# Optimization experiments

Hardware: AMD Instinct MI355X
Metric: run time of the kernel (lower is better)

Reference implementation:

```python
import jax, jax.numpy as jnp
import numpy as np

HS = [192, 96, 48, 24, 12, 6]
WS = [384, 192, 96, 48, 24, 12]
C = 64    # feature channels per pyramid level
F = 64    # num_features (conv output channels)
CIN = 2 * C + 2  # current + warped + 2 flow channels = 130
N = 4


def dense_image_warp(image, flow):
    """tfa.image.dense_image_warp: warped[b,y,x] = bilinear(image[b, y - flow_y, x - flow_x]).
    Boundary handling matches tfa._interpolate_bilinear: floor indices clipped to
    [0, size-2], interpolation alphas clipped to [0, 1]."""
    n, h, w, _ = image.shape
    gy, gx = jnp.meshgrid(jnp.arange(h, dtype=flow.dtype),
                          jnp.arange(w, dtype=flow.dtype), indexing='ij')
    qy = gy[None] - flow[..., 0]          # [N,H,W] query rows
    qx = gx[None] - flow[..., 1]          # [N,H,W] query cols
    y0 = jnp.clip(jnp.floor(qy), 0, h - 2).astype(jnp.int32)
    x0 = jnp.clip(jnp.floor(qx), 0, w - 2).astype(jnp.int32)
    ay = jnp.clip(qy - y0.astype(flow.dtype), 0.0, 1.0)[..., None]
    ax = jnp.clip(qx - x0.astype(flow.dtype), 0.0, 1.0)[..., None]
    b = jnp.arange(n)[:, None, None]
    tl = image[b, y0, x0]
    tr = image[b, y0, x0 + 1]
    bl = image[b, y0 + 1, x0]
    br = image[b, y0 + 1, x0 + 1]
    top = tl + (tr - tl) * ax
    bot = bl + (br - bl) * ax
    return top + (bot - top) * ay


def separable_conv1x1(x, dw, pw, bias):
    # SeparableConv2D with 1x1 kernel: depthwise per-channel scale, then pointwise matmul.
    return jnp.einsum('nhwc,cf->nhwf', x * dw, pw) + bias


def _forward(xcs, xps, fls, dws, pws, bs):
    outs = []
    for i in range(6):
        # _warp: dense_image_warp(x_prev, -flow)
        warped = dense_image_warp(xps[i], -fls[i])
        x = jnp.concatenate([xcs[i], warped, fls[i]], axis=-1)  # [N,H,W,130]
        outs.append(separable_conv1x1(x, dws[i], pws[i], bs[i]))
    return tuple(outs)


def setup_inputs() -> dict:
    key = jax.random.key(0)
    d = {}
    for i in range(6):
        h, w = HS[i], WS[i]
        ks = jax.random.split(jax.random.fold_in(key, i), 6)
        d[f'xc{i}'] = jax.random.normal(ks[0], (N, h, w, C), jnp.float32)
        d[f'xp{i}'] = jax.random.normal(ks[1], (N, h, w, C), jnp.float32)
        d[f'fl{i}'] = jax.random.normal(ks[2], (N, h, w, 2), jnp.float32) * 2.0
        d[f'dw{i}'] = jax.random.normal(ks[3], (CIN,), jnp.float32) * 0.1
        d[f'pw{i}'] = jax.random.normal(ks[4], (CIN, F), jnp.float32) * 0.05
        d[f'bias{i}'] = jnp.zeros((F,), jnp.float32)
    return d


def reference(xc0, xc1, xc2, xc3, xc4, xc5,
              xp0, xp1, xp2, xp3, xp4, xp5,
              fl0, fl1, fl2, fl3, fl4, fl5,
              dw0, dw1, dw2, dw3, dw4, dw5,
              pw0, pw1, pw2, pw3, pw4, pw5,
              bias0, bias1, bias2, bias3, bias4, bias5):
    xcs = (xc0, xc1, xc2, xc3, xc4, xc5)
    xps = (xp0, xp1, xp2, xp3, xp4, xp5)
    fls = (fl0, fl1, fl2, fl3, fl4, fl5)
    dws = (dw0, dw1, dw2, dw3, dw4, dw5)
    pws = (pw0, pw1, pw2, pw3, pw4, pw5)
    bs = (bias0, bias1, bias2, bias3, bias4, bias5)
    return _forward(xcs, xps, fls, dws, pws, bs)
```

## Files before the change

kernel.cpp:

```cpp
#include <hip/hip_runtime.h>


typedef __attribute__((ext_vector_type(8))) short bf16x8;
typedef __attribute__((ext_vector_type(4))) float f32x4;

#define WS_LVL_STRIDE 17408

__device__ inline unsigned rne_bf16_bits(float f) {
  unsigned u = __builtin_bit_cast(unsigned, f);
  u += 0x7fffu + ((u >> 16) & 1u);
  return u >> 16;
}
__device__ inline int pack_bf16x2(float a, float b) {
  return (int)(rne_bf16_bits(a) | (rne_bf16_bits(b) << 16));
}

struct LevelArgs {
  const float* __restrict__ xc;
  const float* __restrict__ xp;
  const float* __restrict__ fl;
  float* __restrict__ out;
  const char* __restrict__ wsl;
  int H, W, npix, block_start;
};
struct KArgs { LevelArgs lv[6]; int total_blocks; };

struct PrepLevel {
  const float* __restrict__ dw;
  const float* __restrict__ pw;
  const float* __restrict__ bias;
  char* __restrict__ wsl;
};
struct PrepArgs { PrepLevel lv[6]; };

__global__ void prep_kernel(PrepArgs pa) {
  const PrepLevel P = pa.lv[blockIdx.x];
  int4* __restrict__ frag = (int4*)P.wsl;
  for (int e = (int)threadIdx.x; e < 1024; e += 256) {
    const int kt = e >> 8;
    const int nt = (e >> 6) & 3;
    const int lane = e & 63;
    const int n = 4 * (lane & 15) + nt;
    const int kb = kt * 32 + ((lane >> 4) & 3) * 8;
    int v[4];
#pragma unroll
    for (int jj = 0; jj < 4; ++jj) {
      const int k0 = kb + jj * 2;
      const float w0 = P.dw[k0] * P.pw[(size_t)k0 * 64 + n];
      const float w1 = P.dw[k0 + 1] * P.pw[(size_t)(k0 + 1) * 64 + n];
      v[jj] = pack_bf16x2(w0, w1);
    }
    frag[e] = make_int4(v[0], v[1], v[2], v[3]);
  }
  float* __restrict__ tab = (float*)(P.wsl + 16384);
  if (threadIdx.x < 64) {
    const int f = (int)threadIdx.x;
    tab[f] = P.bias[f];
    tab[64 + f] = P.dw[128] * P.pw[128 * 64 + f];
    tab[128 + f] = P.dw[129] * P.pw[129 * 64 + f];
  }
}

#define SWZ(r, o) \
  ((((unsigned)(r)) << 7) | (((unsigned)(o)) ^ ((((unsigned)(r)) & 7u) << 4)))

__global__ __launch_bounds__(256, 5) void flowwarp_mfma(KArgs ka) {
  __shared__ __align__(16) char lds_raw[256 * 128];

  const int nb = ka.total_blocks;
  const int chunk = (nb + 7) >> 3;
  const int bp = (int)blockIdx.x;
  const int b = (bp & 7) * chunk + (bp >> 3);
  if (b >= nb) return;

  int Lr = 0;
#pragma unroll
  for (int i = 1; i < 6; ++i) Lr = (b >= ka.lv[i].block_start) ? i : Lr;
  const int L = __builtin_amdgcn_readfirstlane(Lr);
  const LevelArgs A = ka.lv[L];

  const int q = (int)threadIdx.x;
  const int p0 = (b - A.block_start) * 256;
  const int W = A.W, H = A.H;

  float fl0, fl1;

  {
    int p = p0 + q;
    if (p > A.npix - 1) p = A.npix - 1;
    const int x = p % W;
    const int t = p / W;
    const int y = t % H;
    const int n = t / H;

    fl0 = A.fl[2 * (size_t)p];
    fl1 = A.fl[2 * (size_t)p + 1];

    const float qy = (float)y + fl0;
    const float qx = (float)x + fl1;
    const float fy = fminf(fmaxf(floorf(qy), 0.0f), (float)(H - 2));
    const float fx = fminf(fmaxf(floorf(qx), 0.0f), (float)(W - 2));
    const int y0 = (int)fy, x0 = (int)fx;
    const float ay = fminf(fmaxf(qy - fy, 0.0f), 1.0f);
    const float ax = fminf(fmaxf(qx - fx, 0.0f), 1.0f);

    const float* __restrict__ base =
        A.xp + ((size_t)((n * H + y0) * W + x0)) * 64;
    const int W64 = W * 64;
    const f32x4* __restrict__ tl4 = (const f32x4*)base;
    const f32x4* __restrict__ tr4 = (const f32x4*)(base + 64);
    const f32x4* __restrict__ bl4 = (const f32x4*)(base + W64);
    const f32x4* __restrict__ br4 = (const f32x4*)(base + W64 + 64);

#pragma unroll 1
    for (int bq = 0; bq < 4; ++bq) {
      f32x4 rtl[4], rtr[4], rbl[4], rbr[4];
#pragma unroll
      for (int i = 0; i < 4; ++i) {
        rtl[i] = tl4[bq * 4 + i];
        rtr[i] = tr4[bq * 4 + i];
        rbl[i] = bl4[bq * 4 + i];
        rbr[i] = br4[bq * 4 + i];
      }
      int v[8];
#pragma unroll
      for (int i = 0; i < 4; ++i) {
        float wv[4];
#pragma unroll
        for (int j = 0; j < 4; ++j) {
          const float top = fmaf(rtr[i][j] - rtl[i][j], ax, rtl[i][j]);
          const float bot = fmaf(rbr[i][j] - rbl[i][j], ax, rbl[i][j]);
          wv[j] = fmaf(bot - top, ay, top);
        }
        v[i * 2] = pack_bf16x2(wv[0], wv[1]);
        v[i * 2 + 1] = pack_bf16x2(wv[2], wv[3]);
      }
      *(int4*)(lds_raw + SWZ(q, bq * 32)) = make_int4(v[0], v[1], v[2], v[3]);
      *(int4*)(lds_raw + SWZ(q, bq * 32 + 16)) =
          make_int4(v[4], v[5], v[6], v[7]);
    }
  }
  asm volatile("s_waitcnt lgkmcnt(0)" ::: "memory");

  const int lane = q & 63;
  const int w = q >> 6;
  const int m16 = lane & 15;
  const int q4l = lane >> 4;

  const int4* __restrict__ bfr = (const int4*)A.wsl;
  bf16x8 Bf[4][4];
#pragma unroll
  for (int kt = 0; kt < 4; ++kt)
#pragma unroll
    for (int nt = 0; nt < 4; ++nt)
      Bf[kt][nt] = __builtin_bit_cast(bf16x8, bfr[(kt * 4 + nt) * 64 + lane]);

  const float* __restrict__ tab = (const float*)(A.wsl + 16384);
  const f32x4 bvv  = *(const f32x4*)(tab + 4 * m16);
  const f32x4 t0vv = *(const f32x4*)(tab + 64 + 4 * m16);
  const f32x4 t1vv = *(const f32x4*)(tab + 128 + 4 * m16);

  const int npix1 = A.npix - 1;
  int pm = p0 + w * 64 + m16;
  if (pm > npix1) pm = npix1;
  const float* __restrict__ xcp = A.xc + (size_t)pm * 64 + q4l * 8;
  f32x4 na0 = __builtin_nontemporal_load((const f32x4*)xcp);
  f32x4 na1 = __builtin_nontemporal_load((const f32x4*)(xcp + 4));
  f32x4 na2 = __builtin_nontemporal_load((const f32x4*)(xcp + 32));
  f32x4 na3 = __builtin_nontemporal_load((const f32x4*)(xcp + 36));

#pragma unroll 1
  for (int mt = 0; mt < 4; ++mt) {
    const int lrow = w * 64 + mt * 16;
    const f32x4 a0 = na0, a1 = na1, a2 = na2, a3 = na3;
    if (mt < 3) {
      int pn = p0 + lrow + 16 + m16;
      if (pn > npix1) pn = npix1;
      const float* __restrict__ xn = A.xc + (size_t)pn * 64 + q4l * 8;
      na0 = __builtin_nontemporal_load((const f32x4*)xn);
      na1 = __builtin_nontemporal_load((const f32x4*)(xn + 4));
      na2 = __builtin_nontemporal_load((const f32x4*)(xn + 32));
      na3 = __builtin_nontemporal_load((const f32x4*)(xn + 36));
    }
    int av[8];
    av[0] = pack_bf16x2(a0[0], a0[1]); av[1] = pack_bf16x2(a0[2], a0[3]);
    av[2] = pack_bf16x2(a1[0], a1[1]); av[3] = pack_bf16x2(a1[2], a1[3]);
    av[4] = pack_bf16x2(a2[0], a2[1]); av[5] = pack_bf16x2(a2[2], a2[3]);
    av[6] = pack_bf16x2(a3[0], a3[1]); av[7] = pack_bf16x2(a3[2], a3[3]);
    const bf16x8 A0 = __builtin_bit_cast(bf16x8, make_int4(av[0], av[1], av[2], av[3]));
    const bf16x8 A1 = __builtin_bit_cast(bf16x8, make_int4(av[4], av[5], av[6], av[7]));
    const int rr = lrow + m16;
    const bf16x8 A2 = __builtin_bit_cast(
        bf16x8, *(const int4*)(lds_raw + SWZ(rr, q4l * 16)));
    const bf16x8 A3 = __builtin_bit_cast(
        bf16x8, *(const int4*)(lds_raw + SWZ(rr, 64 + q4l * 16)));

    f32x4 acc[4] = {{0.f, 0.f, 0.f, 0.f}, {0.f, 0.f, 0.f, 0.f},
                    {0.f, 0.f, 0.f, 0.f}, {0.f, 0.f, 0.f, 0.f}};
#pragma unroll
    for (int nt = 0; nt < 4; ++nt) {
      acc[nt] = __builtin_amdgcn_mfma_f32_16x16x32_bf16(A0, Bf[0][nt], acc[nt], 0, 0, 0);
      acc[nt] = __builtin_amdgcn_mfma_f32_16x16x32_bf16(A1, Bf[1][nt], acc[nt], 0, 0, 0);
      acc[nt] = __builtin_amdgcn_mfma_f32_16x16x32_bf16(A2, Bf[2][nt], acc[nt], 0, 0, 0);
      acc[nt] = __builtin_amdgcn_mfma_f32_16x16x32_bf16(A3, Bf[3][nt], acc[nt], 0, 0, 0);
    }

#pragma unroll
    for (int i = 0; i < 4; ++i) {
      const int srcl = mt * 16 + q4l * 4 + i;
      const float f0i = __shfl(fl0, srcl);
      const float f1i = __shfl(fl1, srcl);
      const int prow = p0 + lrow + q4l * 4 + i;
      if (prow < A.npix) {
        f32x4 o;
        o[0] = acc[0][i] + bvv[0] + f0i * t0vv[0] + f1i * t1vv[0];
        o[1] = acc[1][i] + bvv[1] + f0i * t0vv[1] + f1i * t1vv[1];
        o[2] = acc[2][i] + bvv[2] + f0i * t0vv[2] + f1i * t1vv[2];
        o[3] = acc[3][i] + bvv[3] + f0i * t1vv[3] * 0.0f + f1i * t1vv[3] +
               f0i * t0vv[3];
        __builtin_nontemporal_store(
            o, (f32x4*)(A.out + (size_t)prow * 64 + 4 * m16));
      }
    }
  }
}

extern "C" void kernel_launch(void* const* d_in, const int* in_sizes, int n_in,
                              void* d_out, int out_size, void* d_ws, size_t ws_size,
                              hipStream_t stream) {
  static const int HS[6] = {192, 96, 48, 24, 12, 6};
  static const int WS[6] = {384, 192, 96, 48, 24, 12};
  PrepArgs pa;
  KArgs ka;
  int bstart = 0;
  size_t ooff = 0;
  for (int i = 0; i < 6; ++i) {
    char* wsl = (char*)d_ws + (size_t)i * WS_LVL_STRIDE;
    pa.lv[i].dw   = (const float*)d_in[6 * i + 3];
    pa.lv[i].pw   = (const float*)d_in[6 * i + 4];
    pa.lv[i].bias = (const float*)d_in[6 * i + 5];
    pa.lv[i].wsl  = wsl;
    ka.lv[i].xc  = (const float*)d_in[6 * i + 0];
    ka.lv[i].xp  = (const float*)d_in[6 * i + 1];
    ka.lv[i].fl  = (const float*)d_in[6 * i + 2];
    ka.lv[i].out = (float*)d_out + ooff;
    ka.lv[i].wsl = wsl;
    const int npix = 4 * HS[i] * WS[i];
    ka.lv[i].H = HS[i];
    ka.lv[i].W = WS[i];
    ka.lv[i].npix = npix;
    ka.lv[i].block_start = bstart;
    bstart += (npix + 255) / 256;
    ooff += (size_t)npix * 64;
  }
  ka.total_blocks = bstart;
  prep_kernel<<<dim3(6), dim3(256), 0, stream>>>(pa);
  const int chunk = (bstart + 7) >> 3;
  flowwarp_mfma<<<dim3(chunk * 8), dim3(256), 0, stream>>>(ka);
}
```

Measured before the change: 426.1 us.

## Cooperative coalesced bilinear gather, drop nontemporal hints on loads/stores

Restructures the warp gather so that groups of 4 lanes cooperatively fetch one pixel's four 256-byte corner rows, with per-pixel offsets and weights broadcast via shuffles, instead of each thread reading a whole 64-channel row. This should make the global loads coalesced across lanes rather than strided per thread, at the cost of extra shuffles and narrower LDS writes. It also replaces the nontemporal loads and stores on xc and out with ordinary ones and removes a redundant multiply-by-zero term in the epilogue.

```diff
diff --git a/kernel.cpp b/kernel.cpp
--- a/kernel.cpp
+++ b/kernel.cpp
@@ -82,6 +82,9 @@
   const int q = (int)threadIdx.x;
   const int p0 = (b - A.block_start) * 256;
   const int W = A.W, H = A.H;
+  const int lane = q & 63;
+  const int w = q >> 6;
+  const int wbase = w * 64;
 
   float fl0, fl1;
 
@@ -103,47 +106,50 @@
     const int y0 = (int)fy, x0 = (int)fx;
     const float ay = fminf(fmaxf(qy - fy, 0.0f), 1.0f);
     const float ax = fminf(fmaxf(qx - fx, 0.0f), 1.0f);
-
-    const float* __restrict__ base =
-        A.xp + ((size_t)((n * H + y0) * W + x0)) * 64;
-    const int W64 = W * 64;
-    const f32x4* __restrict__ tl4 = (const f32x4*)base;
-    const f32x4* __restrict__ tr4 = (const f32x4*)(base + 64);
-    const f32x4* __restrict__ bl4 = (const f32x4*)(base + W64);
-    const f32x4* __restrict__ br4 = (const f32x4*)(base + W64 + 64);
+    const unsigned off = (unsigned)((n * H + y0) * W + x0) * 256u;
+
+    const char* __restrict__ xpb = (const char*)A.xp;
+    const int W256 = W * 256;
+    const int g = lane >> 2;
+    const int s16 = (lane & 3) * 16;
 
 #pragma unroll 1
-    for (int bq = 0; bq < 4; ++bq) {
-      f32x4 rtl[4], rtr[4], rbl[4], rbr[4];
-#pragma unroll
-      for (int i = 0; i < 4; ++i) {
-        rtl[i] = tl4[bq * 4 + i];
-        rtr[i] = tr4[bq * 4 + i];
-        rbl[i] = bl4[bq * 4 + i];
-        rbr[i] = br4[bq * 4 + i];
+    for (int r = 0; r < 4; ++r) {
+      const int src = r * 16 + g;
+      const unsigned offB = (unsigned)__shfl((int)off, src);
+      const float axB = __shfl(ax, src);
+      const float ayB = __shfl(ay, src);
+      const int lrow = wbase + src;
+
+#pragma unroll
+      for (int h = 0; h < 2; ++h) {
+        f32x4 ctl[2], ctr[2], cbl[2], cbr[2];
+#pragma unroll
+        for (int qd = 0; qd < 2; ++qd) {
+          const int o = (h * 2 + qd) * 64 + s16;
+          ctl[qd] = *(const f32x4*)(xpb + offB + o);
+          ctr[qd] = *(const f32x4*)(xpb + offB + 256 + o);
+          cbl[qd] = *(const f32x4*)(xpb + offB + W256 + o);
+          cbr[qd] = *(const f32x4*)(xpb + offB + W256 + 256 + o);
+        }
+#pragma unroll
+        for (int qd = 0; qd < 2; ++qd) {
+          float wv[4];
+#pragma unroll
+          for (int j = 0; j < 4; ++j) {
+            const float top = fmaf(ctr[qd][j] - ctl[qd][j], axB, ctl[qd][j]);
+            const float bot = fmaf(cbr[qd][j] - cbl[qd][j], axB, cbl[qd][j]);
+            wv[j] = fmaf(bot - top, ayB, top);
+          }
+          const int ob = (h * 2 + qd) * 32 + (lane & 3) * 8;
+          *(int2*)(lds_raw + SWZ(lrow, ob)) =
+              make_int2(pack_bf16x2(wv[0], wv[1]), pack_bf16x2(wv[2], wv[3]));
+        }
       }
-      int v[8];
-#pragma unroll
-      for (int i = 0; i < 4; ++i) {
-        float wv[4];
-#pragma unroll
-        for (int j = 0; j < 4; ++j) {
-          const float top = fmaf(rtr[i][j] - rtl[i][j], ax, rtl[i][j]);
-          const float bot = fmaf(rbr[i][j] - rbl[i][j], ax, rbl[i][j]);
-          wv[j] = fmaf(bot - top, ay, top);
-        }
-        v[i * 2] = pack_bf16x2(wv[0], wv[1]);
-        v[i * 2 + 1] = pack_bf16x2(wv[2], wv[3]);
-      }
-      *(int4*)(lds_raw + SWZ(q, bq * 32)) = make_int4(v[0], v[1], v[2], v[3]);
-      *(int4*)(lds_raw + SWZ(q, bq * 32 + 16)) =
-          make_int4(v[4], v[5], v[6], v[7]);
     }
   }
   asm volatile("s_waitcnt lgkmcnt(0)" ::: "memory");
 
-  const int lane = q & 63;
-  const int w = q >> 6;
   const int m16 = lane & 15;
   const int q4l = lane >> 4;
 
@@ -161,26 +167,26 @@
   const f32x4 t1vv = *(const f32x4*)(tab + 128 + 4 * m16);
 
   const int npix1 = A.npix - 1;
-  int pm = p0 + w * 64 + m16;
+  int pm = p0 + wbase + m16;
   if (pm > npix1) pm = npix1;
   const float* __restrict__ xcp = A.xc + (size_t)pm * 64 + q4l * 8;
-  f32x4 na0 = __builtin_nontemporal_load((const f32x4*)xcp);
-  f32x4 na1 = __builtin_nontemporal_load((const f32x4*)(xcp + 4));
-  f32x4 na2 = __builtin_nontemporal_load((const f32x4*)(xcp + 32));
-  f32x4 na3 = __builtin_nontemporal_load((const f32x4*)(xcp + 36));
+  f32x4 na0 = *(const f32x4*)xcp;
+  f32x4 na1 = *(const f32x4*)(xcp + 4);
+  f32x4 na2 = *(const f32x4*)(xcp + 32);
+  f32x4 na3 = *(const f32x4*)(xcp + 36);
 
 #pragma unroll 1
   for (int mt = 0; mt < 4; ++mt) {
-    const int lrow = w * 64 + mt * 16;
+    const int lrow = wbase + mt * 16;
     const f32x4 a0 = na0, a1 = na1, a2 = na2, a3 = na3;
     if (mt < 3) {
       int pn = p0 + lrow + 16 + m16;
       if (pn > npix1) pn = npix1;
       const float* __restrict__ xn = A.xc + (size_t)pn * 64 + q4l * 8;
-      na0 = __builtin_nontemporal_load((const f32x4*)xn);
-      na1 = __builtin_nontemporal_load((const f32x4*)(xn + 4));
-      na2 = __builtin_nontemporal_load((const f32x4*)(xn + 32));
-      na3 = __builtin_nontemporal_load((const f32x4*)(xn + 36));
+      na0 = *(const f32x4*)xn;
+      na1 = *(const f32x4*)(xn + 4);
+      na2 = *(const f32x4*)(xn + 32);
+      na3 = *(const f32x4*)(xn + 36);
     }
     int av[8];
     av[0] = pack_bf16x2(a0[0], a0[1]); av[1] = pack_bf16x2(a0[2], a0[3]);
@@ -216,10 +222,8 @@
         o[0] = acc[0][i] + bvv[0] + f0i * t0vv[0] + f1i * t1vv[0];
         o[1] = acc[1][i] + bvv[1] + f0i * t0vv[1] + f1i * t1vv[1];
         o[2] = acc[2][i] + bvv[2] + f0i * t0vv[2] + f1i * t1vv[2];
-        o[3] = acc[3][i] + bvv[3] + f0i * t1vv[3] * 0.0f + f1i * t1vv[3] +
-               f0i * t0vv[3];
-        __builtin_nontemporal_store(
-            o, (f32x4*)(A.out + (size_t)prow * 64 + 4 * m16));
+        o[3] = acc[3][i] + bvv[3] + f0i * t0vv[3] + f1i * t1vv[3];
+        *(f32x4*)(A.out + (size_t)prow * 64 + 4 * m16) = o;
       }
     }
   }
```

Result: faster. 375.4 us (-11.9%).
